# Kernel optimization log

Hardware: AMD Instinct MI355X
Metric: run time of the kernel (lower is better)

The kernel has to match this reference:

```python
import jax, jax.numpy as jnp
import numpy as np

B, T, C = 4, 4096, 256

def setup_inputs() -> dict:
    key = jax.random.key(0)
    ks = jax.random.split(key, 7)
    s = 1.0 / np.sqrt(C)
    return {
        "x": jax.random.normal(ks[0], (B, T, C), dtype=jnp.float32),
        "Wq": jax.random.uniform(ks[1], (C, C), jnp.float32, -s, s),
        "bq": jax.random.uniform(ks[2], (C,), jnp.float32, -s, s),
        "Wk": jax.random.uniform(ks[3], (C, C), jnp.float32, -s, s),
        "bk": jax.random.uniform(ks[4], (C,), jnp.float32, -s, s),
        "Wv": jax.random.uniform(ks[5], (C, C), jnp.float32, -s, s),
        "bv": jax.random.uniform(ks[6], (C,), jnp.float32, -s, s),
    }

def reference(x, Wq, bq, Wk, bk, Wv, bv):
    # Projections (torch Linear: y = x @ W^T + b; here W stored as [in,out])
    q = x @ Wq + bq  # [B,T,C]
    k = x @ Wk + bk
    v = x @ Wv + bv
    dk = q.shape[-1]
    scores = jnp.einsum('btc,bsc->bts', q, k) / jnp.sqrt(jnp.float32(dk))
    Tn = x.shape[1]
    causal = jnp.tril(jnp.ones((Tn, Tn), dtype=bool))  # [T,T]
    scores = jnp.where(causal[None, :, :], scores, jnp.float32(-1e9))
    attn = jax.nn.softmax(scores, axis=-1)
    return jnp.einsum('bts,bsc->btc', attn, v)
```

## Files before the change

### kernel.cpp

```cpp
#include <hip/hip_runtime.h>
#include <hip/hip_bf16.h>

#define T_SEQ 4096
#define DIM   256
#define NBATCH 4

typedef short s8v __attribute__((ext_vector_type(8)));
typedef float f4v __attribute__((ext_vector_type(4)));
typedef unsigned short u16;

#define MFMA16(a,b,c) __builtin_amdgcn_mfma_f32_16x16x32_bf16(a,b,c,0,0,0)
#define FENCE_LGKM() asm volatile("s_waitcnt lgkmcnt(0)" ::: "memory")

__device__ int g_cnt[4];

static __device__ __forceinline__ u16 f2bf(float f) {
  union { float f; unsigned int u; } c; c.f = f;
  unsigned int u = c.u;
  unsigned int r = (u + 0x7fffu + ((u >> 16) & 1u)) >> 16;
  return (u16)r;
}

static __device__ __forceinline__ s8v pack8(const float* p) {
  float4 a = *(const float4*)p;
  float4 b = *(const float4*)(p + 4);
  s8v r;
  r[0] = (short)f2bf(a.x); r[1] = (short)f2bf(a.y);
  r[2] = (short)f2bf(a.z); r[3] = (short)f2bf(a.w);
  r[4] = (short)f2bf(b.x); r[5] = (short)f2bf(b.y);
  r[6] = (short)f2bf(b.z); r[7] = (short)f2bf(b.w);
  return r;
}

static __device__ __forceinline__ void gll16(const u16* g, u16* l) {
  __builtin_amdgcn_global_load_lds(
      (const __attribute__((address_space(1))) unsigned int*)g,
      (__attribute__((address_space(3))) unsigned int*)l, 16, 0, 0);
}

__global__ void diag_fill_kernel(float* __restrict__ out, float val, int n) {
  int i = blockIdx.x * blockDim.x + threadIdx.x;
  if (i < n) out[i] = val;
}

__global__ void wtrans_kernel(const float* __restrict__ Wq, const float* __restrict__ Wk,
                              const float* __restrict__ Wv, u16* __restrict__ Wt) {
  if (blockIdx.x == 0 && blockIdx.y == 0 && blockIdx.z == 0 &&
      threadIdx.y == 0 && threadIdx.x < 4)
    g_cnt[threadIdx.x] = 0;
  __shared__ float tile[32][33];
  int m = blockIdx.z;
  const float* W = (m == 0) ? Wq : ((m == 1) ? Wk : Wv);
  int bx = blockIdx.x * 32, by = blockIdx.y * 32;
  int x = threadIdx.x, y = threadIdx.y;
  #pragma unroll
  for (int i = 0; i < 32; i += 8) tile[y + i][x] = W[(by + y + i) * DIM + bx + x];
  __syncthreads();
  u16* o = Wt + m * DIM * DIM;
  #pragma unroll
  for (int i = 0; i < 32; i += 8) o[(bx + y + i) * DIM + by + x] = f2bf(tile[x][y + i]);
}

__global__ __launch_bounds__(256) void proj_kernel(
    const float* __restrict__ x, const u16* __restrict__ Wt,
    const float* __restrict__ bk, const float* __restrict__ bv,
    u16* __restrict__ kf, u16* __restrict__ vf) {
  alignas(16) __shared__ u16 Kl[64 * 264];
  alignas(16) __shared__ u16 Vl[256 * 72];

  int bid = blockIdx.x;
  int which = blockIdx.y;
  int tid  = threadIdx.x;
  int wave = tid >> 6, lane = tid & 63, quad = lane >> 4, l16 = lane & 15;
  int row0 = bid * 64 + wave * 16;

  s8v a[8];
  const float* xp = x + (size_t)(row0 + l16) * DIM + quad * 8;
  #pragma unroll
  for (int ks = 0; ks < 8; ks++) a[ks] = pack8(xp + ks * 32);

  if (which == 0) {
    const u16* W = Wt + DIM * DIM;
    f4v acc[16];
    #pragma unroll
    for (int nt = 0; nt < 16; nt++) acc[nt] = (f4v){0.f, 0.f, 0.f, 0.f};
    #pragma unroll
    for (int ks = 0; ks < 8; ks++) {
      #pragma unroll
      for (int nt = 0; nt < 16; nt++) {
        s8v bfr = *(const s8v*)(W + (nt * 16 + l16) * DIM + ks * 32 + quad * 8);
        acc[nt] = MFMA16(a[ks], bfr, acc[nt]);
      }
    }
    #pragma unroll
    for (int nt = 0; nt < 16; nt++) {
      float bb = bk[nt * 16 + l16];
      #pragma unroll
      for (int r = 0; r < 4; r++)
        Kl[(wave * 16 + quad * 4 + r) * 264 + nt * 16 + l16] = f2bf(acc[nt][r] + bb);
    }
    __syncthreads();
    #pragma unroll
    for (int i = 0; i < 8; i++) {
      int o = tid + i * 256;
      int tile = o >> 10, rem = o & 1023;
      int f = rem >> 6, ln = rem & 63;
      int sl = tile * 32 + (f >> 3) * 16 + (ln & 15);
      int c  = (f & 7) * 32 + (ln >> 4) * 8;
      s8v v = *(const s8v*)&Kl[sl * 264 + c];
      *(s8v*)&kf[(((size_t)(bid * 2 + tile) * 16 + f) * 64 + ln) * 8] = v;
    }
  } else {
    const u16* W = Wt + 2 * DIM * DIM;
    f4v acc[16];
    #pragma unroll
    for (int nt = 0; nt < 16; nt++) acc[nt] = (f4v){0.f, 0.f, 0.f, 0.f};
    #pragma unroll
    for (int ks = 0; ks < 8; ks++) {
      #pragma unroll
      for (int nt = 0; nt < 16; nt++) {
        s8v bfr = *(const s8v*)(W + (nt * 16 + l16) * DIM + ks * 32 + quad * 8);
        acc[nt] = MFMA16(a[ks], bfr, acc[nt]);
      }
    }
    #pragma unroll
    for (int nt = 0; nt < 16; nt++) {
      float bb = bv[nt * 16 + l16];
      union { u16 h[4]; uint2 v2; } pk;
      #pragma unroll
      for (int r = 0; r < 4; r++) pk.h[r] = f2bf(acc[nt][r] + bb);
      *(uint2*)&Vl[(nt * 16 + l16) * 72 + wave * 16 + quad * 4] = pk.v2;
    }
    __syncthreads();
    #pragma unroll
    for (int i = 0; i < 8; i++) {
      int o = tid + i * 256;
      int tile = o >> 10, rem = o & 1023;
      int nt = rem >> 6, ln = rem & 63;
      int c  = nt * 16 + (ln & 15);
      int sl = tile * 32 + (ln >> 4) * 8;
      s8v v = *(const s8v*)&Vl[c * 72 + sl];
      *(s8v*)&vf[(((size_t)(bid * 2 + tile) * 16 + nt) * 64 + ln) * 8] = v;
    }
  }
}

__global__ __launch_bounds__(256, 2) void attn_kernel(
    const float* __restrict__ x, const u16* __restrict__ wtq, const float* __restrict__ bq,
    const u16* __restrict__ kf, const u16* __restrict__ vf,
    float* __restrict__ Opart, float* __restrict__ lpart, float* __restrict__ out) {
  alignas(16) __shared__ u16 KV[2][16384];
  alignas(16) __shared__ u16 Ps[4 * 640];
  __shared__ int taskS;
  u16* Qs = &KV[0][0];

  int bid = blockIdx.x;
  int b = bid & 3;
  int tid = threadIdx.x;
  int w = tid >> 6, lane = tid & 63, quad = lane >> 4, l16 = lane & 15;

  const u16* kfb = kf + (size_t)b * 128 * 8192;
  const u16* vfb = vf + (size_t)b * 128 * 8192;

  for (;;) {
    if (tid == 0) taskS = atomicAdd(&g_cnt[b], 1);
    __syncthreads();
    int t = taskS;
    if (t >= 160) break;
    int q64, c;
    if (t < 4)        { q64 = 63; c = t; }
    else if (t < 49)  { int u = t - 4;  q64 = 62 - u / 3; c = u % 3; }
    else if (t < 52)  { q64 = 47; c = t - 49; }
    else if (t < 82)  { int u = t - 52; q64 = 46 - (u >> 1); c = u & 1; }
    else if (t < 84)  { q64 = 31; c = t - 82; }
    else if (t < 99)  { q64 = 30 - (t - 84); c = 0; }
    else if (t == 99) { q64 = 15; c = 0; }
    else { int u = t - 100; int m = u >> 2, g = u & 3, j = 14 - m;
           if (g == 0)      { q64 = 16 + j; c = 1; }
           else if (g == 1) { q64 = 32 + j; c = 2; }
           else if (g == 2) { q64 = 48 + j; c = 3; }
           else             { q64 = j;      c = 0; } }
    int row0 = q64 * 64;
    int n = 2 * q64 + 2;
    int lo = c * 32, hi = min(n, lo + 32);
    int nch = (q64 >> 4) + 1;

    {
      f4v qacc[4][4];
      #pragma unroll
      for (int g2 = 0; g2 < 4; g2++)
        #pragma unroll
        for (int j = 0; j < 4; j++) qacc[g2][j] = (f4v){0.f, 0.f, 0.f, 0.f};
      #pragma unroll
      for (int ks = 0; ks < 8; ks++) {
        s8v wf[4];
        #pragma unroll
        for (int j = 0; j < 4; j++)
          wf[j] = *(const s8v*)(wtq + ((w * 4 + j) * 16 + l16) * DIM + ks * 32 + quad * 8);
        #pragma unroll
        for (int g2 = 0; g2 < 4; g2++) {
          s8v xa = pack8(x + (size_t)(b * T_SEQ + row0 + g2 * 16 + l16) * DIM + ks * 32 + quad * 8);
          #pragma unroll
          for (int j = 0; j < 4; j++) qacc[g2][j] = MFMA16(xa, wf[j], qacc[g2][j]);
        }
      }
      #pragma unroll
      for (int j = 0; j < 4; j++) {
        int nt = w * 4 + j;
        float bb = bq[nt * 16 + l16];
        #pragma unroll
        for (int g2 = 0; g2 < 4; g2++)
          #pragma unroll
          for (int r = 0; r < 4; r++)
            Qs[(g2 * 16 + quad * 4 + r) * 264 + nt * 16 + l16] =
                f2bf((qacc[g2][j][r] + bb) * 0.0625f);
      }
    }
    __syncthreads();
    s8v qa[8];
    #pragma unroll
    for (int ks = 0; ks < 8; ks++)
      qa[ks] = *(const s8v*)&Qs[(w * 16 + l16) * 264 + ks * 32 + quad * 8];
    __syncthreads();

    int rowBase = row0 + w * 16;

    f4v o[16];
    #pragma unroll
    for (int nt = 0; nt < 16; nt++) o[nt] = (f4v){0.f, 0.f, 0.f, 0.f};
    float lrow[4] = {0.f, 0.f, 0.f, 0.f};

    {
      const u16* kt = kfb + ((size_t)lo << 13);
      const u16* vt = vfb + ((size_t)lo << 13);
      #pragma unroll
      for (int i = 0; i < 4; i++) {
        gll16(kt + (w << 11) + (i << 9) + (lane << 3), &KV[0][(w << 11) + (i << 9)]);
        gll16(vt + (w << 11) + (i << 9) + (lane << 3), &KV[0][8192 + (w << 11) + (i << 9)]);
      }
    }
    __syncthreads();

    #pragma unroll 1
    for (int kv = lo; kv < hi; kv++) {
      int cur = (kv - lo) & 1;

      if (kv + 1 < hi) {
        const u16* kt = kfb + ((size_t)(kv + 1) << 13);
        const u16* vt = vfb + ((size_t)(kv + 1) << 13);
        u16* dst = &KV[cur ^ 1][0];
        #pragma unroll
        for (int i = 0; i < 4; i++) {
          gll16(kt + (w << 11) + (i << 9) + (lane << 3), dst + (w << 11) + (i << 9));
          gll16(vt + (w << 11) + (i << 9) + (lane << 3), dst + 8192 + (w << 11) + (i << 9));
        }
      }

      f4v c0 = (f4v){0.f, 0.f, 0.f, 0.f}, c1 = (f4v){0.f, 0.f, 0.f, 0.f};
      {
        s8v kfr[8];
        #pragma unroll
        for (int f = 0; f < 8; f++) kfr[f] = *(const s8v*)&KV[cur][(f << 9) + (lane << 3)];
        #pragma unroll
        for (int ks = 0; ks < 8; ks++) c0 = MFMA16(qa[ks], kfr[ks], c0);
        #pragma unroll
        for (int f = 0; f < 8; f++) kfr[f] = *(const s8v*)&KV[cur][((8 + f) << 9) + (lane << 3)];
        #pragma unroll
        for (int ks = 0; ks < 8; ks++) c1 = MFMA16(qa[ks], kfr[ks], c1);
      }

      int s0 = kv * 32 + l16;
      #pragma unroll
      for (int r = 0; r < 4; r++) {
        int tq = rowBase + quad * 4 + r;
        float v0 = (s0 > tq)      ? -1e30f : c0[r];
        float v1 = (s0 + 16 > tq) ? -1e30f : c1[r];
        float p0 = __expf(v0);
        float p1 = __expf(v1);
        Ps[w * 640 + (quad * 4 + r) * 40 + l16]      = f2bf(p0);
        Ps[w * 640 + (quad * 4 + r) * 40 + 16 + l16] = f2bf(p1);
        lrow[r] += p0 + p1;
      }
      FENCE_LGKM();
      s8v pa = *(const s8v*)&Ps[w * 640 + l16 * 40 + quad * 8];

      {
        s8v vfr[8];
        #pragma unroll
        for (int f = 0; f < 8; f++) vfr[f] = *(const s8v*)&KV[cur][8192 + (f << 9) + (lane << 3)];
        #pragma unroll
        for (int nt = 0; nt < 8; nt++) o[nt] = MFMA16(pa, vfr[nt], o[nt]);
        #pragma unroll
        for (int f = 0; f < 8; f++) vfr[f] = *(const s8v*)&KV[cur][8192 + ((8 + f) << 9) + (lane << 3)];
        #pragma unroll
        for (int nt = 0; nt < 8; nt++) o[8 + nt] = MFMA16(pa, vfr[nt], o[8 + nt]);
      }

      __syncthreads();
    }

    #pragma unroll
    for (int r = 0; r < 4; r++) {
      #pragma unroll
      for (int d = 1; d < 16; d <<= 1) lrow[r] += __shfl_xor(lrow[r], d);
    }

    if (nch == 1) {
      float inv[4];
      #pragma unroll
      for (int r = 0; r < 4; r++) inv[r] = 1.0f / lrow[r];
      #pragma unroll
      for (int nt = 0; nt < 16; nt++) {
        #pragma unroll
        for (int r = 0; r < 4; r++)
          out[(size_t)(b * T_SEQ + rowBase + quad * 4 + r) * DIM + nt * 16 + l16] =
              o[nt][r] * inv[r];
      }
    } else {
      int slotB = (q64 < 32) ? (q64 - 16) * 2
                : (q64 < 48) ? 32 + (q64 - 32) * 3
                             : 80 + (q64 - 48) * 4;
      int slot = b * 144 + slotB + c;
      float* Op = Opart + ((size_t)slot << 14);
      #pragma unroll
      for (int nt = 0; nt < 16; nt++) {
        #pragma unroll
        for (int r = 0; r < 4; r++)
          Op[(w * 16 + quad * 4 + r) * 256 + nt * 16 + l16] = o[nt][r];
      }
      if (l16 == 0) {
        #pragma unroll
        for (int r = 0; r < 4; r++)
          lpart[slot * 64 + w * 16 + quad * 4 + r] = lrow[r];
      }
    }
  }
}

__global__ void combine_kernel(const float* __restrict__ Opart,
                               const float* __restrict__ lpart,
                               float* __restrict__ out) {
  int blk = blockIdx.x;
  int b = blk & 3;
  int rest = blk >> 2;
  int q64 = 16 + (rest >> 2);
  int g = rest & 3;
  int col = threadIdx.x;
  int nch = (q64 >> 4) + 1;
  int slotB = (q64 < 32) ? (q64 - 16) * 2
            : (q64 < 48) ? 32 + (q64 - 32) * 3
                         : 80 + (q64 - 48) * 4;
  int slot0 = b * 144 + slotB;
  #pragma unroll 4
  for (int i = 0; i < 16; i++) {
    int rt = g * 16 + i;
    float acc = 0.f, ls = 0.f;
    for (int c = 0; c < nch; c++) {
      acc += Opart[(((size_t)(slot0 + c)) << 14) + rt * 256 + col];
      ls  += lpart[(slot0 + c) * 64 + rt];
    }
    out[(size_t)(b * T_SEQ + q64 * 64 + rt) * DIM + col] = acc / ls;
  }
}

extern "C" void kernel_launch(void* const* d_in, const int* in_sizes, int n_in,
                              void* d_out, int out_size, void* d_ws, size_t ws_size,
                              hipStream_t stream) {
  const float* x  = (const float*)d_in[0];
  const float* Wq = (const float*)d_in[1];
  const float* bq = (const float*)d_in[2];
  const float* Wk = (const float*)d_in[3];
  const float* bk = (const float*)d_in[4];
  const float* Wv = (const float*)d_in[5];
  const float* bv = (const float*)d_in[6];

  const size_t NTD = (size_t)NBATCH * T_SEQ * DIM;
  const size_t WT_ELEMS = (size_t)3 * DIM * DIM;
  const size_t NSLOT = 576;
  const size_t REQ_BYTES = (WT_ELEMS + 2 * NTD) * sizeof(u16)
                         + NSLOT * 16384 * sizeof(float)
                         + NSLOT * 64 * sizeof(float);

  if (ws_size < REQ_BYTES) {
    float val = (float)(ws_size >> 20);
    diag_fill_kernel<<<(out_size + 255) / 256, 256, 0, stream>>>((float*)d_out, val, out_size);
    return;
  }

  u16* ws = (u16*)d_ws;
  u16* WT = ws;
  u16* Kf = ws + WT_ELEMS;
  u16* Vf = Kf + NTD;
  float* Opart = (float*)(Vf + NTD);
  float* lpart = Opart + NSLOT * 16384;

  wtrans_kernel<<<dim3(8, 8, 3), dim3(32, 8, 1), 0, stream>>>(Wq, Wk, Wv, WT);
  proj_kernel<<<dim3(256, 2, 1), dim3(256, 1, 1), 0, stream>>>(x, WT, bk, bv, Kf, Vf);
  attn_kernel<<<dim3(512, 1, 1), dim3(256, 1, 1), 0, stream>>>(x, WT, bq, Kf, Vf,
                                                               Opart, lpart, (float*)d_out);
  combine_kernel<<<dim3(768, 1, 1), dim3(256, 1, 1), 0, stream>>>(Opart, lpart, (float*)d_out);
}
```

Baseline: 242.0 us.

## Precompute Q in projection kernel and use 128-row, 16-wave attention tiles

Q projection moves out of the attention kernel into proj_kernel, which writes a bf16 Q buffer with a rotated column layout to reduce LDS bank conflicts. The attention kernel now processes 128 query rows per 1024-thread block, with wave pairs splitting the V output columns. This lets each K/V tile loaded into shared memory serve twice as many query rows, and Q fragments are read from LDS on each use. Double buffering uses explicit A/B buffers, and the task schedule and combine slots are rebuilt for 128-row tiles. The cost is more shared memory per block, an extra Q round-trip through global memory, and lower block-level parallelism.

Measured after the change: 227.9 us. -5.8%, faster.

```diff
diff --git a/kernel.cpp b/kernel.cpp
--- a/kernel.cpp
+++ b/kernel.cpp
@@ -63,8 +63,8 @@
 
 __global__ __launch_bounds__(256) void proj_kernel(
     const float* __restrict__ x, const u16* __restrict__ Wt,
-    const float* __restrict__ bk, const float* __restrict__ bv,
-    u16* __restrict__ kf, u16* __restrict__ vf) {
+    const float* __restrict__ bq, const float* __restrict__ bk, const float* __restrict__ bv,
+    u16* __restrict__ qf, u16* __restrict__ kf, u16* __restrict__ vf) {
   alignas(16) __shared__ u16 Kl[64 * 264];
   alignas(16) __shared__ u16 Vl[256 * 72];
 
@@ -110,7 +110,7 @@
       s8v v = *(const s8v*)&Kl[sl * 264 + c];
       *(s8v*)&kf[(((size_t)(bid * 2 + tile) * 16 + f) * 64 + ln) * 8] = v;
     }
-  } else {
+  } else if (which == 1) {
     const u16* W = Wt + 2 * DIM * DIM;
     f4v acc[16];
     #pragma unroll
@@ -142,160 +142,153 @@
       s8v v = *(const s8v*)&Vl[c * 72 + sl];
       *(s8v*)&vf[(((size_t)(bid * 2 + tile) * 16 + nt) * 64 + ln) * 8] = v;
     }
+  } else {
+    const u16* W = Wt;
+    f4v acc[16];
+    #pragma unroll
+    for (int nt = 0; nt < 16; nt++) acc[nt] = (f4v){0.f, 0.f, 0.f, 0.f};
+    #pragma unroll
+    for (int ks = 0; ks < 8; ks++) {
+      #pragma unroll
+      for (int nt = 0; nt < 16; nt++) {
+        s8v bfr = *(const s8v*)(W + (nt * 16 + l16) * DIM + ks * 32 + quad * 8);
+        acc[nt] = MFMA16(a[ks], bfr, acc[nt]);
+      }
+    }
+    #pragma unroll
+    for (int nt = 0; nt < 16; nt++) {
+      float bb = bq[nt * 16 + l16];
+      #pragma unroll
+      for (int r = 0; r < 4; r++)
+        Kl[(wave * 16 + quad * 4 + r) * 264 + nt * 16 + l16] =
+            f2bf((acc[nt][r] + bb) * 0.0625f);
+    }
+    __syncthreads();
+    #pragma unroll
+    for (int i = 0; i < 8; i++) {
+      int o = tid + i * 256;
+      int row = o >> 5, c8 = (o & 31) * 8;
+      s8v v = *(const s8v*)&Kl[row * 264 + c8];
+      int colp = (c8 + ((row & 31) << 3)) & 255;
+      *(s8v*)&qf[(size_t)(bid * 64 + row) * 256 + colp] = v;
+    }
   }
 }
 
-__global__ __launch_bounds__(256, 2) void attn_kernel(
-    const float* __restrict__ x, const u16* __restrict__ wtq, const float* __restrict__ bq,
-    const u16* __restrict__ kf, const u16* __restrict__ vf,
+__global__ __launch_bounds__(1024, 4) void attn_kernel(
+    const u16* __restrict__ qf, const u16* __restrict__ kf, const u16* __restrict__ vf,
     float* __restrict__ Opart, float* __restrict__ lpart, float* __restrict__ out) {
-  alignas(16) __shared__ u16 KV[2][16384];
-  alignas(16) __shared__ u16 Ps[4 * 640];
+  alignas(16) __shared__ u16 Qs[32768];
+  alignas(16) __shared__ u16 KVa[16384];
+  alignas(16) __shared__ u16 KVb[16384];
+  alignas(16) __shared__ u16 Ps[16 * 640];
   __shared__ int taskS;
-  u16* Qs = &KV[0][0];
-
-  int bid = blockIdx.x;
-  int b = bid & 3;
+
+  int bid = blockIdx.x, b = bid & 3;
   int tid = threadIdx.x;
   int w = tid >> 6, lane = tid & 63, quad = lane >> 4, l16 = lane & 15;
-
+  int s = w >> 1, h = w & 1;
+
+  const u16* qfb = qf + (size_t)b * T_SEQ * DIM;
   const u16* kfb = kf + (size_t)b * 128 * 8192;
   const u16* vfb = vf + (size_t)b * 128 * 8192;
 
+  int qrow = (s << 4) + l16;
+  int qbase = qrow << 8;
+  int qrot = (qrow & 31) << 3;
+
   for (;;) {
     if (tid == 0) taskS = atomicAdd(&g_cnt[b], 1);
     __syncthreads();
     int t = taskS;
-    if (t >= 160) break;
-    int q64, c;
-    if (t < 4)        { q64 = 63; c = t; }
-    else if (t < 49)  { int u = t - 4;  q64 = 62 - u / 3; c = u % 3; }
-    else if (t < 52)  { q64 = 47; c = t - 49; }
-    else if (t < 82)  { int u = t - 52; q64 = 46 - (u >> 1); c = u & 1; }
-    else if (t < 84)  { q64 = 31; c = t - 82; }
-    else if (t < 99)  { q64 = 30 - (t - 84); c = 0; }
-    else if (t == 99) { q64 = 15; c = 0; }
-    else { int u = t - 100; int m = u >> 2, g = u & 3, j = 14 - m;
-           if (g == 0)      { q64 = 16 + j; c = 1; }
-           else if (g == 1) { q64 = 32 + j; c = 2; }
-           else if (g == 2) { q64 = 48 + j; c = 3; }
-           else             { q64 = j;      c = 0; } }
-    int row0 = q64 * 64;
-    int n = 2 * q64 + 2;
+    if (t >= 80) break;
+    int q, c;
+    if (t < 8)        { q = 24 + t;        c = 0; }
+    else if (t < 16)  { q = 24 + (t - 8);  c = 1; }
+    else if (t < 24)  { q = 24 + (t - 16); c = 2; }
+    else if (t == 24) { q = 31;            c = 3; }
+    else if (t < 33)  { q = 16 + (t - 25); c = 0; }
+    else if (t < 41)  { q = 16 + (t - 33); c = 1; }
+    else if (t == 41) { q = 23;            c = 2; }
+    else if (t < 50)  { q = 8 + (t - 42);  c = 0; }
+    else if (t == 50) { q = 15;            c = 1; }
+    else if (t == 51) { q = 7;             c = 0; }
+    else { int u = t - 52, sz = u >> 2, band = u & 3;
+           if (band == 0)      { q = 6 - sz;  c = 0; }
+           else if (band == 1) { q = 14 - sz; c = 1; }
+           else if (band == 2) { q = 22 - sz; c = 2; }
+           else                { q = 30 - sz; c = 3; } }
+    int row0 = q * 128;
+    int n = 4 * q + 4;
     int lo = c * 32, hi = min(n, lo + 32);
-    int nch = (q64 >> 4) + 1;
+    int nch = (q + 8) >> 3;
 
     {
-      f4v qacc[4][4];
-      #pragma unroll
-      for (int g2 = 0; g2 < 4; g2++)
-        #pragma unroll
-        for (int j = 0; j < 4; j++) qacc[g2][j] = (f4v){0.f, 0.f, 0.f, 0.f};
-      #pragma unroll
-      for (int ks = 0; ks < 8; ks++) {
-        s8v wf[4];
-        #pragma unroll
-        for (int j = 0; j < 4; j++)
-          wf[j] = *(const s8v*)(wtq + ((w * 4 + j) * 16 + l16) * DIM + ks * 32 + quad * 8);
-        #pragma unroll
-        for (int g2 = 0; g2 < 4; g2++) {
-          s8v xa = pack8(x + (size_t)(b * T_SEQ + row0 + g2 * 16 + l16) * DIM + ks * 32 + quad * 8);
-          #pragma unroll
-          for (int j = 0; j < 4; j++) qacc[g2][j] = MFMA16(xa, wf[j], qacc[g2][j]);
-        }
-      }
-      #pragma unroll
-      for (int j = 0; j < 4; j++) {
-        int nt = w * 4 + j;
-        float bb = bq[nt * 16 + l16];
-        #pragma unroll
-        for (int g2 = 0; g2 < 4; g2++)
-          #pragma unroll
-          for (int r = 0; r < 4; r++)
-            Qs[(g2 * 16 + quad * 4 + r) * 264 + nt * 16 + l16] =
-                f2bf((qacc[g2][j][r] + bb) * 0.0625f);
-      }
-    }
-    __syncthreads();
-    s8v qa[8];
-    #pragma unroll
-    for (int ks = 0; ks < 8; ks++)
-      qa[ks] = *(const s8v*)&Qs[(w * 16 + l16) * 264 + ks * 32 + quad * 8];
-    __syncthreads();
-
-    int rowBase = row0 + w * 16;
-
-    f4v o[16];
-    #pragma unroll
-    for (int nt = 0; nt < 16; nt++) o[nt] = (f4v){0.f, 0.f, 0.f, 0.f};
-    float lrow[4] = {0.f, 0.f, 0.f, 0.f};
-
-    {
+      const u16* qsrc = qfb + ((size_t)row0 << 8) + (w << 11) + (lane << 3);
+      u16* qdst = &Qs[w << 11];
+      #pragma unroll
+      for (int i = 0; i < 4; i++) gll16(qsrc + (i << 9), qdst + (i << 9));
       const u16* kt = kfb + ((size_t)lo << 13);
       const u16* vt = vfb + ((size_t)lo << 13);
-      #pragma unroll
-      for (int i = 0; i < 4; i++) {
-        gll16(kt + (w << 11) + (i << 9) + (lane << 3), &KV[0][(w << 11) + (i << 9)]);
-        gll16(vt + (w << 11) + (i << 9) + (lane << 3), &KV[0][8192 + (w << 11) + (i << 9)]);
-      }
-    }
-    __syncthreads();
-
-    #pragma unroll 1
-    for (int kv = lo; kv < hi; kv++) {
-      int cur = (kv - lo) & 1;
-
-      if (kv + 1 < hi) {
-        const u16* kt = kfb + ((size_t)(kv + 1) << 13);
-        const u16* vt = vfb + ((size_t)(kv + 1) << 13);
-        u16* dst = &KV[cur ^ 1][0];
-        #pragma unroll
-        for (int i = 0; i < 4; i++) {
-          gll16(kt + (w << 11) + (i << 9) + (lane << 3), dst + (w << 11) + (i << 9));
-          gll16(vt + (w << 11) + (i << 9) + (lane << 3), dst + 8192 + (w << 11) + (i << 9));
-        }
-      }
-
+      gll16(kt + (w << 9) + (lane << 3), &KVa[w << 9]);
+      gll16(vt + (w << 9) + (lane << 3), &KVa[8192 + (w << 9)]);
+    }
+    __syncthreads();
+
+    int rowBase = row0 + (s << 4);
+    f4v o[8];
+    #pragma unroll
+    for (int nt = 0; nt < 8; nt++) o[nt] = (f4v){0.f, 0.f, 0.f, 0.f};
+    float lrow[4] = {0.f, 0.f, 0.f, 0.f};
+
+    auto iter_body = [&](const u16* buf, int kvi) {
       f4v c0 = (f4v){0.f, 0.f, 0.f, 0.f}, c1 = (f4v){0.f, 0.f, 0.f, 0.f};
-      {
-        s8v kfr[8];
-        #pragma unroll
-        for (int f = 0; f < 8; f++) kfr[f] = *(const s8v*)&KV[cur][(f << 9) + (lane << 3)];
-        #pragma unroll
-        for (int ks = 0; ks < 8; ks++) c0 = MFMA16(qa[ks], kfr[ks], c0);
-        #pragma unroll
-        for (int f = 0; f < 8; f++) kfr[f] = *(const s8v*)&KV[cur][((8 + f) << 9) + (lane << 3)];
-        #pragma unroll
-        for (int ks = 0; ks < 8; ks++) c1 = MFMA16(qa[ks], kfr[ks], c1);
-      }
-
-      int s0 = kv * 32 + l16;
+      #pragma unroll
+      for (int ks = 0; ks < 8; ks++) {
+        s8v qa = *(const s8v*)&Qs[qbase + ((ks * 32 + (quad << 3) + qrot) & 255)];
+        s8v k0 = *(const s8v*)&buf[(ks << 9) + (lane << 3)];
+        s8v k1 = *(const s8v*)&buf[((8 + ks) << 9) + (lane << 3)];
+        c0 = MFMA16(qa, k0, c0);
+        c1 = MFMA16(qa, k1, c1);
+      }
+      int s0 = kvi * 32 + l16;
       #pragma unroll
       for (int r = 0; r < 4; r++) {
-        int tq = rowBase + quad * 4 + r;
+        int tq = rowBase + (quad << 2) + r;
         float v0 = (s0 > tq)      ? -1e30f : c0[r];
         float v1 = (s0 + 16 > tq) ? -1e30f : c1[r];
         float p0 = __expf(v0);
         float p1 = __expf(v1);
-        Ps[w * 640 + (quad * 4 + r) * 40 + l16]      = f2bf(p0);
-        Ps[w * 640 + (quad * 4 + r) * 40 + 16 + l16] = f2bf(p1);
+        Ps[w * 640 + ((quad << 2) + r) * 40 + l16]      = f2bf(p0);
+        Ps[w * 640 + ((quad << 2) + r) * 40 + 16 + l16] = f2bf(p1);
         lrow[r] += p0 + p1;
       }
       FENCE_LGKM();
-      s8v pa = *(const s8v*)&Ps[w * 640 + l16 * 40 + quad * 8];
-
+      s8v pa = *(const s8v*)&Ps[w * 640 + l16 * 40 + (quad << 3)];
+      #pragma unroll
+      for (int nt = 0; nt < 8; nt++) {
+        s8v vfr = *(const s8v*)&buf[8192 + (((h << 3) + nt) << 9) + (lane << 3)];
+        o[nt] = MFMA16(pa, vfr, o[nt]);
+      }
+    };
+
+    #pragma unroll 1
+    for (int kv = lo; kv < hi; kv += 2) {
       {
-        s8v vfr[8];
-        #pragma unroll
-        for (int f = 0; f < 8; f++) vfr[f] = *(const s8v*)&KV[cur][8192 + (f << 9) + (lane << 3)];
-        #pragma unroll
-        for (int nt = 0; nt < 8; nt++) o[nt] = MFMA16(pa, vfr[nt], o[nt]);
-        #pragma unroll
-        for (int f = 0; f < 8; f++) vfr[f] = *(const s8v*)&KV[cur][8192 + ((8 + f) << 9) + (lane << 3)];
-        #pragma unroll
-        for (int nt = 0; nt < 8; nt++) o[8 + nt] = MFMA16(pa, vfr[nt], o[8 + nt]);
-      }
-
+        const u16* kt = kfb + ((size_t)(kv + 1) << 13);
+        const u16* vt = vfb + ((size_t)(kv + 1) << 13);
+        gll16(kt + (w << 9) + (lane << 3), &KVb[w << 9]);
+        gll16(vt + (w << 9) + (lane << 3), &KVb[8192 + (w << 9)]);
+      }
+      iter_body(KVa, kv);
+      __syncthreads();
+      if (kv + 2 < hi) {
+        const u16* kt = kfb + ((size_t)(kv + 2) << 13);
+        const u16* vt = vfb + ((size_t)(kv + 2) << 13);
+        gll16(kt + (w << 9) + (lane << 3), &KVa[w << 9]);
+        gll16(vt + (w << 9) + (lane << 3), &KVa[8192 + (w << 9)]);
+      }
+      iter_body(KVb, kv + 1);
       __syncthreads();
     }
 
@@ -310,28 +303,28 @@
       #pragma unroll
       for (int r = 0; r < 4; r++) inv[r] = 1.0f / lrow[r];
       #pragma unroll
-      for (int nt = 0; nt < 16; nt++) {
+      for (int nt = 0; nt < 8; nt++) {
         #pragma unroll
         for (int r = 0; r < 4; r++)
-          out[(size_t)(b * T_SEQ + rowBase + quad * 4 + r) * DIM + nt * 16 + l16] =
-              o[nt][r] * inv[r];
+          out[(size_t)(b * T_SEQ + rowBase + (quad << 2) + r) * DIM +
+              ((h * 8 + nt) * 16 + l16)] = o[nt][r] * inv[r];
       }
     } else {
-      int slotB = (q64 < 32) ? (q64 - 16) * 2
-                : (q64 < 48) ? 32 + (q64 - 32) * 3
-                             : 80 + (q64 - 48) * 4;
-      int slot = b * 144 + slotB + c;
-      float* Op = Opart + ((size_t)slot << 14);
-      #pragma unroll
-      for (int nt = 0; nt < 16; nt++) {
+      int slotB = (q < 16) ? (q - 8) * 2
+                : (q < 24) ? 16 + (q - 16) * 3
+                           : 40 + (q - 24) * 4;
+      int slot = b * 72 + slotB + c;
+      float* Op = Opart + ((size_t)slot << 15);
+      #pragma unroll
+      for (int nt = 0; nt < 8; nt++) {
         #pragma unroll
         for (int r = 0; r < 4; r++)
-          Op[(w * 16 + quad * 4 + r) * 256 + nt * 16 + l16] = o[nt][r];
-      }
-      if (l16 == 0) {
+          Op[((s << 4) + (quad << 2) + r) * 256 + (h * 8 + nt) * 16 + l16] = o[nt][r];
+      }
+      if (h == 0 && l16 == 0) {
         #pragma unroll
         for (int r = 0; r < 4; r++)
-          lpart[slot * 64 + w * 16 + quad * 4 + r] = lrow[r];
+          lpart[slot * 128 + (s << 4) + (quad << 2) + r] = lrow[r];
       }
     }
   }
@@ -343,23 +336,23 @@
   int blk = blockIdx.x;
   int b = blk & 3;
   int rest = blk >> 2;
-  int q64 = 16 + (rest >> 2);
-  int g = rest & 3;
+  int q = 8 + (rest >> 3);
+  int g = rest & 7;
   int col = threadIdx.x;
-  int nch = (q64 >> 4) + 1;
-  int slotB = (q64 < 32) ? (q64 - 16) * 2
-            : (q64 < 48) ? 32 + (q64 - 32) * 3
-                         : 80 + (q64 - 48) * 4;
-  int slot0 = b * 144 + slotB;
+  int nch = (q + 8) >> 3;
+  int slotB = (q < 16) ? (q - 8) * 2
+            : (q < 24) ? 16 + (q - 16) * 3
+                       : 40 + (q - 24) * 4;
+  int slot0 = b * 72 + slotB;
   #pragma unroll 4
   for (int i = 0; i < 16; i++) {
     int rt = g * 16 + i;
     float acc = 0.f, ls = 0.f;
     for (int c = 0; c < nch; c++) {
-      acc += Opart[(((size_t)(slot0 + c)) << 14) + rt * 256 + col];
-      ls  += lpart[(slot0 + c) * 64 + rt];
-    }
-    out[(size_t)(b * T_SEQ + q64 * 64 + rt) * DIM + col] = acc / ls;
+      acc += Opart[(((size_t)(slot0 + c)) << 15) + rt * 256 + col];
+      ls  += lpart[(slot0 + c) * 128 + rt];
+    }
+    out[(size_t)(b * T_SEQ + q * 128 + rt) * DIM + col] = acc / ls;
   }
 }
 
@@ -376,10 +369,10 @@
 
   const size_t NTD = (size_t)NBATCH * T_SEQ * DIM;
   const size_t WT_ELEMS = (size_t)3 * DIM * DIM;
-  const size_t NSLOT = 576;
-  const size_t REQ_BYTES = (WT_ELEMS + 2 * NTD) * sizeof(u16)
-                         + NSLOT * 16384 * sizeof(float)
-                         + NSLOT * 64 * sizeof(float);
+  const size_t NSLOT = 288;
+  const size_t REQ_BYTES = (WT_ELEMS + 3 * NTD) * sizeof(u16)
+                         + NSLOT * 32768 * sizeof(float)
+                         + NSLOT * 128 * sizeof(float);
 
   if (ws_size < REQ_BYTES) {
     float val = (float)(ws_size >> 20);
@@ -391,12 +384,13 @@
   u16* WT = ws;
   u16* Kf = ws + WT_ELEMS;
   u16* Vf = Kf + NTD;
-  float* Opart = (float*)(Vf + NTD);
-  float* lpart = Opart + NSLOT * 16384;
+  u16* Qf = Vf + NTD;
+  float* Opart = (float*)(Qf + NTD);
+  float* lpart = Opart + NSLOT * 32768;
 
   wtrans_kernel<<<dim3(8, 8, 3), dim3(32, 8, 1), 0, stream>>>(Wq, Wk, Wv, WT);
-  proj_kernel<<<dim3(256, 2, 1), dim3(256, 1, 1), 0, stream>>>(x, WT, bk, bv, Kf, Vf);
-  attn_kernel<<<dim3(512, 1, 1), dim3(256, 1, 1), 0, stream>>>(x, WT, bq, Kf, Vf,
-                                                               Opart, lpart, (float*)d_out);
+  proj_kernel<<<dim3(256, 3, 1), dim3(256, 1, 1), 0, stream>>>(x, WT, bq, bk, bv, Qf, Kf, Vf);
+  attn_kernel<<<dim3(256, 1, 1), dim3(1024, 1, 1), 0, stream>>>(Qf, Kf, Vf,
+                                                                Opart, lpart, (float*)d_out);
   combine_kernel<<<dim3(768, 1, 1), dim3(256, 1, 1), 0, stream>>>(Opart, lpart, (float*)d_out);
 }
```
